# Performance work log

Measured on AMD Instinct MI355X. Metric: run time of the kernel, lower is better.

The kernel has to match this reference:

```python
import jax, jax.numpy as jnp
import numpy as np

IN_DIM = 300
MEM_DIM = 1024
DEPTH = 14  # perfect binary tree in heap order: N = 2**DEPTH - 1 = 16383 nodes


def _init_linear(key, out_dim, in_dim):
    # torch nn.Linear default init: U(-1/sqrt(in), 1/sqrt(in)) for W and b
    s = 1.0 / np.sqrt(in_dim)
    kw, kb = jax.random.split(key)
    W = jax.random.uniform(kw, (out_dim, in_dim), jnp.float32, -s, s)
    b = jax.random.uniform(kb, (out_dim,), jnp.float32, -s, s)
    return W, b


def setup_inputs() -> dict:
    key = jax.random.key(0)
    keys = jax.random.split(key, 9)
    N = 2 ** DEPTH - 1
    inp = {"embs": jax.random.normal(keys[0], (N, IN_DIM), jnp.float32)}
    gates = [("ix", IN_DIM), ("ih", MEM_DIM), ("fx", IN_DIM), ("fh", MEM_DIM),
             ("ox", IN_DIM), ("oh", MEM_DIM), ("ux", IN_DIM), ("uh", MEM_DIM)]
    for k, (name, d) in zip(keys[1:], gates):
        W, b = _init_linear(k, MEM_DIM, d)
        inp["W" + name] = W
        inp["b" + name] = b
    inp["depth"] = DEPTH
    return inp


def _lin(x, W, b):
    return x @ W.T + b


def reference(embs, Wix, bix, Wih, bih, Wfx, bfx, Wfh, bfh,
              Wox, box, Woh, boh, Wux, bux, Wuh, buh, depth):
    # Child-Sum TreeLSTM on a perfect binary tree (heap order), processed
    # bottom-up, batching all nodes of a level into single GEMMs.
    h = c = None
    for lvl in range(depth - 1, -1, -1):
        n = 2 ** lvl
        x = embs[n - 1:2 * n - 1]  # [n, in_dim], nodes of this level
        if h is None:
            # leaves: original code feeds a single zero child -> h_sum = 0
            # and f * child_c = 0 regardless of f
            hsum = jnp.zeros((n, MEM_DIM), embs.dtype)
            fc = jnp.zeros((n, MEM_DIM), embs.dtype)
        else:
            hc = h.reshape(n, 2, MEM_DIM)  # children hidden states
            cc = c.reshape(n, 2, MEM_DIM)  # children cell states
            hsum = hc.sum(axis=1)
            # per-child forget gate: sigmoid(fh(h_k) + fx(x))
            f = jax.nn.sigmoid(jnp.einsum('nkd,md->nkm', hc, Wfh) + bfh
                               + _lin(x, Wfx, bfx)[:, None, :])
            fc = (f * cc).sum(axis=1)
        i = jax.nn.sigmoid(_lin(x, Wix, bix) + _lin(hsum, Wih, bih))
        o = jax.nn.sigmoid(_lin(x, Wox, box) + _lin(hsum, Woh, boh))
        u = jnp.tanh(_lin(x, Wux, bux) + _lin(hsum, Wuh, buh))
        c = i * u + fc
        h = o * jnp.tanh(c)
    return jnp.stack([c[0], h[0]])  # root state (c, h): [2, MEM_DIM]
```

## Files before the change

kernel.cpp:

```cpp
#include <hip/hip_runtime.h>
#include <hip/hip_bf16.h>

#define IN_DIM 300
#define XDIM   320
#define MEM    1024
#define NTREE  16383

typedef _Float16 half8 __attribute__((ext_vector_type(8)));
typedef float    f32x4 __attribute__((ext_vector_type(4)));

__device__ __forceinline__ float sigf(float x) { return 1.0f / (1.0f + __expf(-x)); }
__device__ __forceinline__ float tanhfast(float x) { return 2.0f / (1.0f + __expf(-2.0f * x)) - 1.0f; }

#define GLOAD_LDS16(g, l) \
    __builtin_amdgcn_global_load_lds((const __attribute__((address_space(1))) void*)(g), \
                                     (__attribute__((address_space(3))) void*)(l), 16, 0, 0)

__global__ void pack_kernel(
    const float* __restrict__ embs,
    const float* __restrict__ Wix, const float* __restrict__ bix,
    const float* __restrict__ Wih, const float* __restrict__ bih,
    const float* __restrict__ Wfx, const float* __restrict__ bfx,
    const float* __restrict__ Wfh, const float* __restrict__ bfh,
    const float* __restrict__ Wox, const float* __restrict__ box_,
    const float* __restrict__ Woh, const float* __restrict__ boh,
    const float* __restrict__ Wux, const float* __restrict__ bux,
    const float* __restrict__ Wuh, const float* __restrict__ buh,
    _Float16* __restrict__ Wiou16, _Float16* __restrict__ Wfh16,
    _Float16* __restrict__ x16, _Float16* __restrict__ Bx)
{
    long long idx = (long long)blockIdx.x * blockDim.x + threadIdx.x;
    const long long n_wiou = 3072LL * 1024;
    const long long n_wfh  = 1024LL * 1024;
    const long long n_x    = 16384LL * XDIM;
    const long long n_bx   = 4096LL * XDIM;
    if (idx < n_wiou) {
        int m = (int)(idx >> 10), k = (int)(idx & 1023);
        int g = m >> 10, mm = m & 1023;
        const float* W = (g == 0) ? Wih : (g == 1) ? Woh : Wuh;
        Wiou16[idx] = (_Float16)W[(long long)mm * MEM + k];
        return;
    }
    idx -= n_wiou;
    if (idx < n_wfh) {
        Wfh16[idx] = (_Float16)Wfh[idx];
        return;
    }
    idx -= n_wfh;
    if (idx < n_x) {
        int node = (int)(idx / XDIM), j = (int)(idx % XDIM);
        float v = 0.f;
        if (node < NTREE) {
            if (j < IN_DIM) v = embs[(long long)node * IN_DIM + j];
            else if (j == IN_DIM) v = 1.0f;
        }
        x16[idx] = (_Float16)v;
        return;
    }
    idx -= n_x;
    if (idx < n_bx) {
        int r = (int)(idx / XDIM), j = (int)(idx % XDIM);
        int g = r >> 10, mm = r & 1023;
        const float* Wx = (g == 0) ? Wix : (g == 1) ? Wox : (g == 2) ? Wux : Wfx;
        const float* b1 = (g == 0) ? bix : (g == 1) ? box_ : (g == 2) ? bux : bfx;
        const float* b2 = (g == 0) ? bih : (g == 1) ? boh : (g == 2) ? buh : bfh;
        float v = 0.f;
        if (j < IN_DIM) v = Wx[(long long)mm * IN_DIM + j];
        else if (j == IN_DIM) v = b1[mm] + b2[mm];
        Bx[idx] = (_Float16)v;
    }
}

template<int BM, int BN, int BK>
__device__ __forceinline__ void gemm_tile(
    const _Float16* __restrict__ A, int lda,
    const _Float16* __restrict__ B, int ldb,
    _Float16* __restrict__ C, int ldc, int K,
    _Float16* ldsA, _Float16* ldsB)
{
    constexpr int FM = BM / 32, FN = BN / 32;
    constexpr int CPR = BK / 8, SWM = CPR - 1;
    constexpr int ACH = BM * BK / 2048, BCH = BN * BK / 2048;

    int tid = threadIdx.x, wave = tid >> 6, lane = tid & 63;
    int wr = (wave >> 1) * (BM / 2), wc = (wave & 1) * (BN / 2);
    int kq = (lane >> 4) * 8, rs = lane & 15;
    f32x4 acc[FM][FN] = {};

    for (int k0 = 0; k0 < K; k0 += BK) {
#pragma unroll
        for (int j = 0; j < ACH; ++j) {
            int c = j * 256 + tid;
            int row = c / CPR;
            int s = (c ^ row) & SWM;
            GLOAD_LDS16(A + (long long)row * lda + k0 + s * 8,
                        &ldsA[(j * 256 + wave * 64) * 8]);
        }
#pragma unroll
        for (int j = 0; j < BCH; ++j) {
            int c = j * 256 + tid;
            int row = c / CPR;
            int s = (c ^ row) & SWM;
            GLOAD_LDS16(B + (long long)row * ldb + k0 + s * 8,
                        &ldsB[(j * 256 + wave * 64) * 8]);
        }
        __syncthreads();
#pragma unroll
        for (int kk = 0; kk < BK; kk += 32) {
            half8 a[FM], b[FN];
#pragma unroll
            for (int i = 0; i < FM; ++i) {
                int r = wr + i * 16 + rs;
                int s = ((kk + kq) >> 3) ^ (r & SWM);
                a[i] = *(const half8*)&ldsA[r * BK + s * 8];
            }
#pragma unroll
            for (int i = 0; i < FN; ++i) {
                int r = wc + i * 16 + rs;
                int s = ((kk + kq) >> 3) ^ (r & SWM);
                b[i] = *(const half8*)&ldsB[r * BK + s * 8];
            }
#pragma unroll
            for (int mi = 0; mi < FM; ++mi)
#pragma unroll
                for (int ni = 0; ni < FN; ++ni)
                    acc[mi][ni] = __builtin_amdgcn_mfma_f32_16x16x32_f16(a[mi], b[ni], acc[mi][ni], 0, 0, 0);
        }
        __syncthreads();
    }
    int crb = wr + (lane >> 4) * 4, ccb = wc + rs;
#pragma unroll
    for (int mi = 0; mi < FM; ++mi)
#pragma unroll
        for (int i = 0; i < 4; ++i) {
            long long r = crb + mi * 16 + i;
#pragma unroll
            for (int ni = 0; ni < FN; ++ni)
                C[r * ldc + ccb + ni * 16] = (_Float16)acc[mi][ni][i];
        }
}

template<int BM, int BN, int BK>
__global__ __launch_bounds__(256) void gemm_f16(
    const _Float16* __restrict__ A, int lda,
    const _Float16* __restrict__ B, int ldb,
    _Float16* __restrict__ C, int ldc, int K)
{
    __shared__ __align__(16) _Float16 ldsA[BM * BK];
    __shared__ __align__(16) _Float16 ldsB[BN * BK];
    gemm_tile<BM, BN, BK>(A + (long long)blockIdx.x * BM * lda, lda,
                          B + (long long)blockIdx.y * BN * ldb, ldb,
                          C + (long long)blockIdx.x * BM * ldc + (long long)blockIdx.y * BN,
                          ldc, K, ldsA, ldsB);
}

template<int BM1, int BM2, int BK>
__global__ __launch_bounds__(256) void gemm_level(
    const _Float16* __restrict__ Hsum, const _Float16* __restrict__ Hc,
    const _Float16* __restrict__ Wiou, const _Float16* __restrict__ Wf,
    _Float16* __restrict__ houpre, _Float16* __restrict__ fpre,
    int G1, int G2)
{
    constexpr int BMX = (BM1 > BM2) ? BM1 : BM2;
    __shared__ __align__(16) _Float16 ldsA[BMX * BK];
    __shared__ __align__(16) _Float16 ldsB[128 * BK];
    int bx = blockIdx.x;
    if (bx < G1 * 24) {
        int nb = bx / G1, mb = bx % G1;
        gemm_tile<BM1, 128, BK>(Hsum + (long long)mb * BM1 * 1024, 1024,
                                Wiou + (long long)nb * 128 * 1024, 1024,
                                houpre + (long long)mb * BM1 * 3072 + nb * 128, 3072,
                                1024, ldsA, ldsB);
    } else {
        int b2 = bx - G1 * 24;
        int nb = b2 / G2, mb = b2 % G2;
        gemm_tile<BM2, 128, BK>(Hc + (long long)mb * BM2 * 1024, 1024,
                                Wf + (long long)nb * 128 * 1024, 1024,
                                fpre + (long long)mb * BM2 * 1024 + nb * 128, 1024,
                                1024, ldsA, ldsB);
    }
}

__global__ __launch_bounds__(256) void leaf_fused(
    const _Float16* __restrict__ x16, const _Float16* __restrict__ Bx,
    _Float16* __restrict__ cleaf, _Float16* __restrict__ hleaf,
    _Float16* __restrict__ hsum)
{
    constexpr int BK = 32, CPR = 4, SWM = 3;
    __shared__ __align__(16) _Float16 lA[64 * BK];
    __shared__ __align__(16) _Float16 lB[384 * BK];
    int tid = threadIdx.x, wave = tid >> 6, lane = tid & 63;
    int kq = (lane >> 4) * 8, rs = lane & 15;
    int wr = (wave >> 1) * 32, wc = (wave & 1) * 64;
    int m0 = blockIdx.x * 64, c0 = blockIdx.y * 128;
    const _Float16* A = x16 + (size_t)(8191 + m0) * XDIM;

    f32x4 acc[3][2][4] = {};
    for (int t = 0; t < 10; ++t) {
        int k0 = t * BK;
        {
            int c = tid, row = c / CPR, s = (c ^ row) & SWM;
            GLOAD_LDS16(A + (long long)row * XDIM + k0 + s * 8, &lA[(wave * 64) * 8]);
        }
#pragma unroll
        for (int j = 0; j < 6; ++j) {
            int c = j * 256 + tid;
            int row = c / CPR, s = (c ^ row) & SWM;
            int g = row >> 7, rr = row & 127;
            GLOAD_LDS16(Bx + (long long)(g * 1024 + c0 + rr) * XDIM + k0 + s * 8,
                        &lB[(j * 256 + wave * 64) * 8]);
        }
        __syncthreads();
        half8 a[2], b[3][4];
#pragma unroll
        for (int mi = 0; mi < 2; ++mi) {
            int r = wr + mi * 16 + rs;
            int s = (kq >> 3) ^ (r & SWM);
            a[mi] = *(const half8*)&lA[r * BK + s * 8];
        }
#pragma unroll
        for (int g = 0; g < 3; ++g)
#pragma unroll
            for (int nj = 0; nj < 4; ++nj) {
                int r = g * 128 + wc + nj * 16 + rs;
                int s = (kq >> 3) ^ (r & SWM);
                b[g][nj] = *(const half8*)&lB[r * BK + s * 8];
            }
#pragma unroll
        for (int g = 0; g < 3; ++g)
#pragma unroll
            for (int mi = 0; mi < 2; ++mi)
#pragma unroll
                for (int nj = 0; nj < 4; ++nj)
                    acc[g][mi][nj] = __builtin_amdgcn_mfma_f32_16x16x32_f16(a[mi], b[g][nj], acc[g][mi][nj], 0, 0, 0);
        __syncthreads();
    }
    int lrb = wr + (lane >> 4) * 4;
#pragma unroll
    for (int mi = 0; mi < 2; ++mi)
#pragma unroll
        for (int nj = 0; nj < 4; ++nj) {
            int col = c0 + wc + nj * 16 + rs;
            float hpair = 0.f;
#pragma unroll
            for (int i = 0; i < 4; ++i) {
                long long l = m0 + lrb + mi * 16 + i;
                float cc = sigf(acc[0][mi][nj][i]) * tanhfast(acc[2][mi][nj][i]);
                float hh = sigf(acc[1][mi][nj][i]) * tanhfast(cc);
                cleaf[l * 1024 + col] = (_Float16)cc;
                hleaf[l * 1024 + col] = (_Float16)hh;
                if (i & 1) hsum[(l >> 1) * 1024 + col] = (_Float16)(hpair + hh);
                else hpair = hh;
            }
        }
}

__global__ void combine_level(
    const _Float16* __restrict__ houpre, const _Float16* __restrict__ fpre,
    const _Float16* __restrict__ cprev,
    const _Float16* __restrict__ Xp,
    _Float16* __restrict__ cout, _Float16* __restrict__ hout, _Float16* __restrict__ hsum,
    int n, int gx0, float* __restrict__ fin)
{
    int idx = blockIdx.x * blockDim.x + threadIdx.x;
    int npairs = (n > 1) ? (n >> 1) : 1;
    if (idx >= npairs * 128) return;
    int r = idx >> 7, m8 = (idx & 127) * 8;
    float hs[8];
#pragma unroll
    for (int j = 0; j < 8; ++j) hs[j] = 0.f;
    int pmax = (n > 1) ? 2 : 1;
    for (int t = 0; t < pmax; ++t) {
        int p = 2 * r + t;
        long long node = gx0 + p;
        half8 phi = *(const half8*)&houpre[(long long)p * 3072 + m8];
        half8 pho = *(const half8*)&houpre[(long long)p * 3072 + 1024 + m8];
        half8 phu = *(const half8*)&houpre[(long long)p * 3072 + 2048 + m8];
        half8 pxi = *(const half8*)&Xp[node * 4096 + m8];
        half8 pxo = *(const half8*)&Xp[node * 4096 + 1024 + m8];
        half8 pxu = *(const half8*)&Xp[node * 4096 + 2048 + m8];
        half8 pxf = *(const half8*)&Xp[node * 4096 + 3072 + m8];
        half8 pf0 = *(const half8*)&fpre[(long long)(2 * p) * 1024 + m8];
        half8 pf1 = *(const half8*)&fpre[(long long)(2 * p + 1) * 1024 + m8];
        half8 pc0 = *(const half8*)&cprev[(long long)(2 * p) * 1024 + m8];
        half8 pc1 = *(const half8*)&cprev[(long long)(2 * p + 1) * 1024 + m8];
        float cw[8], hw[8];
#pragma unroll
        for (int j = 0; j < 8; ++j) {
            float i  = sigf((float)phi[j] + (float)pxi[j]);
            float o  = sigf((float)pho[j] + (float)pxo[j]);
            float u  = tanhfast((float)phu[j] + (float)pxu[j]);
            float f0 = sigf((float)pf0[j] + (float)pxf[j]);
            float f1 = sigf((float)pf1[j] + (float)pxf[j]);
            float c = i * u + f0 * (float)pc0[j] + f1 * (float)pc1[j];
            float h = o * tanhfast(c);
            cw[j] = c; hw[j] = h; hs[j] += h;
        }
        if (fin) {
            f32x4 v0 = {cw[0], cw[1], cw[2], cw[3]}, v1 = {cw[4], cw[5], cw[6], cw[7]};
            f32x4 w0 = {hw[0], hw[1], hw[2], hw[3]}, w1 = {hw[4], hw[5], hw[6], hw[7]};
            *(f32x4*)&fin[m8] = v0;            *(f32x4*)&fin[m8 + 4] = v1;
            *(f32x4*)&fin[1024 + m8] = w0;     *(f32x4*)&fin[1024 + m8 + 4] = w1;
        } else {
            half8 cv, hv;
#pragma unroll
            for (int j = 0; j < 8; ++j) { cv[j] = (_Float16)cw[j]; hv[j] = (_Float16)hw[j]; }
            *(half8*)&cout[(long long)p * 1024 + m8] = cv;
            *(half8*)&hout[(long long)p * 1024 + m8] = hv;
        }
    }
    if (!fin) {
        half8 sv;
#pragma unroll
        for (int j = 0; j < 8; ++j) sv[j] = (_Float16)hs[j];
        *(half8*)&hsum[(long long)r * 1024 + m8] = sv;
    }
}

extern "C" void kernel_launch(void* const* d_in, const int* in_sizes, int n_in,
                              void* d_out, int out_size, void* d_ws, size_t ws_size,
                              hipStream_t stream)
{
    const float* embs = (const float*)d_in[0];
    const float* Wix = (const float*)d_in[1];  const float* bix = (const float*)d_in[2];
    const float* Wih = (const float*)d_in[3];  const float* bih = (const float*)d_in[4];
    const float* Wfx = (const float*)d_in[5];  const float* bfx = (const float*)d_in[6];
    const float* Wfh = (const float*)d_in[7];  const float* bfh = (const float*)d_in[8];
    const float* Wox = (const float*)d_in[9];  const float* box_ = (const float*)d_in[10];
    const float* Woh = (const float*)d_in[11]; const float* boh = (const float*)d_in[12];
    const float* Wux = (const float*)d_in[13]; const float* bux = (const float*)d_in[14];
    const float* Wuh = (const float*)d_in[15]; const float* buh = (const float*)d_in[16];

    char* p = (char*)d_ws;
    auto carve = [&](size_t bytes) -> char* {
        char* r = p; p += (bytes + 255) & ~(size_t)255; return r;
    };
    _Float16* Wiou16 = (_Float16*)carve((size_t)3072 * 1024 * 2);
    _Float16* Wfh16  = (_Float16*)carve((size_t)1024 * 1024 * 2);
    _Float16* Xp     = (_Float16*)carve((size_t)8192 * 4096 * 2);
    _Float16* houpre = (_Float16*)carve((size_t)4096 * 3072 * 2);
    _Float16* fpre   = (_Float16*)carve((size_t)8192 * 1024 * 2);
    _Float16* H_A    = (_Float16*)carve((size_t)8192 * 1024 * 2);
    _Float16* H_B    = (_Float16*)carve((size_t)4096 * 1024 * 2);
    _Float16* HsumA  = (_Float16*)carve((size_t)4096 * 1024 * 2);
    _Float16* HsumB  = (_Float16*)carve((size_t)4096 * 1024 * 2);
    _Float16* Cleaf  = (_Float16*)carve((size_t)8192 * 1024 * 2);
    _Float16* CpingH = (_Float16*)carve((size_t)4096 * 1024 * 2);
    _Float16* CpongH = (_Float16*)carve((size_t)2048 * 1024 * 2);
    _Float16* x16 = fpre;
    _Float16* Bx  = fpre + (size_t)16384 * XDIM;

    {
        long long tot = 3072LL * 1024 + 1024LL * 1024 + 16384LL * XDIM + 4096LL * XDIM;
        pack_kernel<<<dim3((int)((tot + 255) / 256)), dim3(256), 0, stream>>>(
            embs, Wix, bix, Wih, bih, Wfx, bfx, Wfh, bfh,
            Wox, box_, Woh, boh, Wux, bux, Wuh, buh,
            Wiou16, Wfh16, x16, Bx);
    }

    gemm_f16<128, 128, 32><<<dim3(64, 32), dim3(256), 0, stream>>>(
        x16, XDIM, Bx, XDIM, Xp, 4096, XDIM);
    leaf_fused<<<dim3(128, 8), dim3(256), 0, stream>>>(x16, Bx, Cleaf, H_A, HsumA);

    const _Float16* cprev = Cleaf;
    _Float16* cbufs[2] = {CpingH, CpongH};
    _Float16* hsums[2] = {HsumA, HsumB};
    int ci = 0, si = 0;
    _Float16* hcur = H_A;
    _Float16* hnext = H_B;

    for (int lvl = 12; lvl >= 0; --lvl) {
        int n = 1 << lvl;
        int G1, G2;
        if (n >= 1024) {
            G1 = n / 128; G2 = 2 * n / 128;
            gemm_level<128, 128, 32><<<dim3(G1 * 24 + G2 * 8), dim3(256), 0, stream>>>(
                hsums[si], hcur, Wiou16, Wfh16, houpre, fpre, G1, G2);
        } else if (n >= 128) {
            G1 = n / 128; G2 = 2 * n / 128;
            gemm_level<128, 128, 128><<<dim3(G1 * 24 + G2 * 8), dim3(256), 0, stream>>>(
                hsums[si], hcur, Wiou16, Wfh16, houpre, fpre, G1, G2);
        } else if (n == 64) {
            G1 = 1; G2 = 1;
            gemm_level<64, 128, 256><<<dim3(G1 * 24 + G2 * 8), dim3(256), 0, stream>>>(
                hsums[si], hcur, Wiou16, Wfh16, houpre, fpre, G1, G2);
        } else {
            G1 = 1; G2 = 1;
            gemm_level<64, 64, 256><<<dim3(G1 * 24 + G2 * 8), dim3(256), 0, stream>>>(
                hsums[si], hcur, Wiou16, Wfh16, houpre, fpre, G1, G2);
        }

        int npairs = (n > 1) ? (n >> 1) : 1;
        int blocks = (npairs * 128 + 255) / 256;
        float* fin = (lvl == 0) ? (float*)d_out : nullptr;
        combine_level<<<dim3(blocks), dim3(256), 0, stream>>>(
            houpre, fpre, cprev, Xp, cbufs[ci], hnext, hsums[si ^ 1], n, n - 1, fin);

        cprev = cbufs[ci];
        ci ^= 1; si ^= 1;
        _Float16* tmp = hcur; hcur = hnext; hnext = tmp;
    }
}
```

Measured before the change: 438.0 us.

## Split-K the small tail levels of the tree GEMM and reduce partials in combine

For the levels with 64 or fewer nodes, the K=1024 dimension of the hidden-state GEMMs is split into four 256-wide slices. This launches 128 blocks instead of 32, and each slice writes fp16 partial sums to separate buffers. A new combine kernel sums the four partials before applying the gate nonlinearities. The aim is to fill more compute units on the latency-bound tail levels, at the cost of extra partial-sum traffic and an additional fp16 rounding step per slice.

```diff
diff --git a/kernel.cpp b/kernel.cpp
--- a/kernel.cpp
+++ b/kernel.cpp
@@ -181,6 +181,110 @@
     }
 }
 
+__global__ __launch_bounds__(256) void tail_sk(
+    const _Float16* __restrict__ Hsum, const _Float16* __restrict__ Hc,
+    const _Float16* __restrict__ Wiou, const _Float16* __restrict__ Wf,
+    _Float16* __restrict__ houp, _Float16* __restrict__ fp)
+{
+    __shared__ __align__(16) _Float16 ldsA[128 * 256];
+    __shared__ __align__(16) _Float16 ldsB[128 * 256];
+    int bx = blockIdx.x;
+    int s = bx >> 5, r = bx & 31;
+    int k0 = s * 256;
+    if (r < 24) {
+        gemm_tile<64, 128, 256>(Hsum + k0, 1024,
+                                Wiou + (long long)r * 128 * 1024 + k0, 1024,
+                                houp + (long long)s * 64 * 3072 + r * 128, 3072,
+                                256, ldsA, ldsB);
+    } else {
+        int nb = r - 24;
+        gemm_tile<128, 128, 256>(Hc + k0, 1024,
+                                 Wf + (long long)nb * 128 * 1024 + k0, 1024,
+                                 fp + (long long)s * 128 * 1024 + nb * 128, 1024,
+                                 256, ldsA, ldsB);
+    }
+}
+
+__global__ void combine_tail_sk(
+    const _Float16* __restrict__ houp,
+    const _Float16* __restrict__ fp,
+    const _Float16* __restrict__ cprev,
+    const _Float16* __restrict__ Xp,
+    _Float16* __restrict__ cout, _Float16* __restrict__ hout, _Float16* __restrict__ hsum,
+    int n, int gx0, float* __restrict__ fin)
+{
+    int idx = blockIdx.x * blockDim.x + threadIdx.x;
+    int npairs = (n > 1) ? (n >> 1) : 1;
+    if (idx >= npairs * 128) return;
+    int r = idx >> 7, m8 = (idx & 127) * 8;
+    float hs[8];
+#pragma unroll
+    for (int j = 0; j < 8; ++j) hs[j] = 0.f;
+    int pmax = (n > 1) ? 2 : 1;
+    for (int t = 0; t < pmax; ++t) {
+        int p = 2 * r + t;
+        long long node = gx0 + p;
+        float gi[8], go[8], gu[8], q0[8], q1[8];
+        half8 pxi = *(const half8*)&Xp[node * 4096 + m8];
+        half8 pxo = *(const half8*)&Xp[node * 4096 + 1024 + m8];
+        half8 pxu = *(const half8*)&Xp[node * 4096 + 2048 + m8];
+        half8 pxf = *(const half8*)&Xp[node * 4096 + 3072 + m8];
+#pragma unroll
+        for (int j = 0; j < 8; ++j) {
+            gi[j] = (float)pxi[j]; go[j] = (float)pxo[j]; gu[j] = (float)pxu[j];
+            q0[j] = (float)pxf[j]; q1[j] = (float)pxf[j];
+        }
+#pragma unroll
+        for (int s = 0; s < 4; ++s) {
+            const _Float16* hb = houp + ((long long)s * 64 + p) * 3072;
+            half8 a = *(const half8*)&hb[m8];
+            half8 b = *(const half8*)&hb[1024 + m8];
+            half8 c = *(const half8*)&hb[2048 + m8];
+            const _Float16* f0b = fp + ((long long)s * 128 + 2 * p) * 1024;
+            const _Float16* f1b = fp + ((long long)s * 128 + 2 * p + 1) * 1024;
+            half8 d = *(const half8*)&f0b[m8];
+            half8 e = *(const half8*)&f1b[m8];
+#pragma unroll
+            for (int j = 0; j < 8; ++j) {
+                gi[j] += (float)a[j]; go[j] += (float)b[j]; gu[j] += (float)c[j];
+                q0[j] += (float)d[j]; q1[j] += (float)e[j];
+            }
+        }
+        half8 pc0 = *(const half8*)&cprev[(long long)(2 * p) * 1024 + m8];
+        half8 pc1 = *(const half8*)&cprev[(long long)(2 * p + 1) * 1024 + m8];
+        float cw[8], hw[8];
+#pragma unroll
+        for (int j = 0; j < 8; ++j) {
+            float i  = sigf(gi[j]);
+            float o  = sigf(go[j]);
+            float u  = tanhfast(gu[j]);
+            float f0 = sigf(q0[j]);
+            float f1 = sigf(q1[j]);
+            float c = i * u + f0 * (float)pc0[j] + f1 * (float)pc1[j];
+            float h = o * tanhfast(c);
+            cw[j] = c; hw[j] = h; hs[j] += h;
+        }
+        if (fin) {
+            f32x4 v0 = {cw[0], cw[1], cw[2], cw[3]}, v1 = {cw[4], cw[5], cw[6], cw[7]};
+            f32x4 w0 = {hw[0], hw[1], hw[2], hw[3]}, w1 = {hw[4], hw[5], hw[6], hw[7]};
+            *(f32x4*)&fin[m8] = v0;            *(f32x4*)&fin[m8 + 4] = v1;
+            *(f32x4*)&fin[1024 + m8] = w0;     *(f32x4*)&fin[1024 + m8 + 4] = w1;
+        } else {
+            half8 cv, hv;
+#pragma unroll
+            for (int j = 0; j < 8; ++j) { cv[j] = (_Float16)cw[j]; hv[j] = (_Float16)hw[j]; }
+            *(half8*)&cout[(long long)p * 1024 + m8] = cv;
+            *(half8*)&hout[(long long)p * 1024 + m8] = hv;
+        }
+    }
+    if (!fin) {
+        half8 sv;
+#pragma unroll
+        for (int j = 0; j < 8; ++j) sv[j] = (_Float16)hs[j];
+        *(half8*)&hsum[(long long)r * 1024 + m8] = sv;
+    }
+}
+
 __global__ __launch_bounds__(256) void leaf_fused(
     const _Float16* __restrict__ x16, const _Float16* __restrict__ Bx,
     _Float16* __restrict__ cleaf, _Float16* __restrict__ hleaf,
@@ -347,6 +451,8 @@
     _Float16* Cleaf  = (_Float16*)carve((size_t)8192 * 1024 * 2);
     _Float16* CpingH = (_Float16*)carve((size_t)4096 * 1024 * 2);
     _Float16* CpongH = (_Float16*)carve((size_t)2048 * 1024 * 2);
+    _Float16* houp4  = (_Float16*)carve((size_t)4 * 64 * 3072 * 2);
+    _Float16* fp4    = (_Float16*)carve((size_t)4 * 128 * 1024 * 2);
     _Float16* x16 = fpre;
     _Float16* Bx  = fpre + (size_t)16384 * XDIM;
 
@@ -371,30 +477,28 @@
 
     for (int lvl = 12; lvl >= 0; --lvl) {
         int n = 1 << lvl;
-        int G1, G2;
-        if (n >= 1024) {
-            G1 = n / 128; G2 = 2 * n / 128;
-            gemm_level<128, 128, 32><<<dim3(G1 * 24 + G2 * 8), dim3(256), 0, stream>>>(
-                hsums[si], hcur, Wiou16, Wfh16, houpre, fpre, G1, G2);
-        } else if (n >= 128) {
-            G1 = n / 128; G2 = 2 * n / 128;
-            gemm_level<128, 128, 128><<<dim3(G1 * 24 + G2 * 8), dim3(256), 0, stream>>>(
-                hsums[si], hcur, Wiou16, Wfh16, houpre, fpre, G1, G2);
-        } else if (n == 64) {
-            G1 = 1; G2 = 1;
-            gemm_level<64, 128, 256><<<dim3(G1 * 24 + G2 * 8), dim3(256), 0, stream>>>(
-                hsums[si], hcur, Wiou16, Wfh16, houpre, fpre, G1, G2);
-        } else {
-            G1 = 1; G2 = 1;
-            gemm_level<64, 64, 256><<<dim3(G1 * 24 + G2 * 8), dim3(256), 0, stream>>>(
-                hsums[si], hcur, Wiou16, Wfh16, houpre, fpre, G1, G2);
-        }
-
         int npairs = (n > 1) ? (n >> 1) : 1;
         int blocks = (npairs * 128 + 255) / 256;
         float* fin = (lvl == 0) ? (float*)d_out : nullptr;
-        combine_level<<<dim3(blocks), dim3(256), 0, stream>>>(
-            houpre, fpre, cprev, Xp, cbufs[ci], hnext, hsums[si ^ 1], n, n - 1, fin);
+
+        if (n >= 1024) {
+            int G1 = n / 128, G2 = 2 * n / 128;
+            gemm_level<128, 128, 32><<<dim3(G1 * 24 + G2 * 8), dim3(256), 0, stream>>>(
+                hsums[si], hcur, Wiou16, Wfh16, houpre, fpre, G1, G2);
+            combine_level<<<dim3(blocks), dim3(256), 0, stream>>>(
+                houpre, fpre, cprev, Xp, cbufs[ci], hnext, hsums[si ^ 1], n, n - 1, fin);
+        } else if (n >= 128) {
+            int G1 = n / 128, G2 = 2 * n / 128;
+            gemm_level<128, 128, 128><<<dim3(G1 * 24 + G2 * 8), dim3(256), 0, stream>>>(
+                hsums[si], hcur, Wiou16, Wfh16, houpre, fpre, G1, G2);
+            combine_level<<<dim3(blocks), dim3(256), 0, stream>>>(
+                houpre, fpre, cprev, Xp, cbufs[ci], hnext, hsums[si ^ 1], n, n - 1, fin);
+        } else {
+            tail_sk<<<dim3(128), dim3(256), 0, stream>>>(
+                hsums[si], hcur, Wiou16, Wfh16, houp4, fp4);
+            combine_tail_sk<<<dim3(blocks), dim3(256), 0, stream>>>(
+                houp4, fp4, cprev, Xp, cbufs[ci], hnext, hsums[si ^ 1], n, n - 1, fin);
+        }
 
         cprev = cbufs[ci];
         ci ^= 1; si ^= 1;
```

Measured after the change: 464.5 us. +6.0%, slower.
